# Performance work log

Hardware: AMD Instinct MI355X
Metric: run time of the kernel (lower is better)

## Reference

```python
import jax, jax.numpy as jnp
import numpy as np

IN_FEATURES = 3
CODE_NUM = 64
CODE_CHANNEL = 64
SHAPE_NUM = 1


def setup_inputs() -> dict:
    key = jax.random.key(0)
    k1, k2 = jax.random.split(key)
    coords = jax.random.uniform(k1, (8, 65536, IN_FEATURES), dtype=jnp.float32)  # in [0,1) subset of [-1,1]
    table_size = SHAPE_NUM * CODE_NUM ** IN_FEATURES
    # xavier_uniform for [C, N] matrix
    limit = float(np.sqrt(6.0 / (CODE_CHANNEL + table_size)))
    shape_code = jax.random.uniform(k2, (CODE_CHANNEL, table_size), dtype=jnp.float32,
                                    minval=-limit, maxval=limit)
    return {"coords": coords, "shape_code": shape_code, "idx": 0}


def reference(coords, shape_code, idx):
    D = IN_FEATURES
    # corner offset mask: [2^D, D] of {0,1}
    mask = jnp.stack(jnp.meshgrid(*([jnp.arange(2, dtype=jnp.float32)] * D), indexing="ij"), -1)
    mask = mask.reshape(-1, D)                                   # [8, 3]
    mul = jnp.asarray([CODE_NUM ** i for i in range(D)], dtype=jnp.int64)
    offset = jnp.asarray(idx, dtype=jnp.int64) * (CODE_NUM ** D)

    c = (coords + 1.0) * ((CODE_NUM - 1) / 2.0)                  # [B, P, 3] in [0, code_num-1]
    corners = jnp.floor(c)[..., None, :] + mask                  # [B, P, 8, 3]
    coordsf = c[..., None, :] - corners                          # [B, P, 8, 3]
    index = jnp.sum(corners.astype(jnp.int64) * mul, axis=-1) + offset  # [B, P, 8]
    weights = jnp.prod(1.0 - jnp.abs(coordsf), axis=-1)          # [B, P, 8]

    code = jnp.take(shape_code, index, axis=1)                   # [C, B, P, 8] gather
    out = jnp.einsum("cbpk,bpk->bpc", code, weights)             # weighted corner sum
    return out
```

## Files before the change

### kernel.cpp

```cpp
#include <hip/hip_runtime.h>


#define CODE_NUM 64
#define CODE_CHANNEL 64
#define TABLE (CODE_NUM * CODE_NUM * CODE_NUM)
#define NBINS 4096
#define SCAT_PTS 1024
#define SCAT_PPT 4

__global__ __launch_bounds__(256) void init_k(int* __restrict__ hist, int* __restrict__ bbox) {
    const int t = blockIdx.x * 256 + threadIdx.x;
    for (int i = t; i < NBINS; i += gridDim.x * 256) hist[i] = 0;
    if (t == 0) {
        bbox[0] = 0x7fffffff; bbox[1] = (int)0x80000000;
        bbox[2] = 0x7fffffff; bbox[3] = (int)0x80000000;
    }
}

__device__ __forceinline__ int cell_bin(float x, float y, float z,
                                        int& ix, int& iy, int& iz) {
    ix = (int)floorf((x + 1.0f) * ((CODE_NUM - 1) * 0.5f));
    iy = (int)floorf((y + 1.0f) * ((CODE_NUM - 1) * 0.5f));
    iz = (int)floorf((z + 1.0f) * ((CODE_NUM - 1) * 0.5f));
    const int cx = min(max(ix, 0), 63) >> 2;
    const int cy = min(max(iy, 0), 63) >> 2;
    const int cz = min(max(iz, 0), 63) >> 2;
    return cx | (cy << 4) | (cz << 8);
}

__global__ __launch_bounds__(256) void hist_bbox_k(const float* __restrict__ coords, int npoints,
                                                   int* __restrict__ hist, int* __restrict__ bbox) {
    __shared__ int lh[NBINS];
    __shared__ int lb[4];
    for (int i = threadIdx.x; i < NBINS; i += 256) lh[i] = 0;
    if (threadIdx.x == 0) {
        lb[0] = 0x7fffffff; lb[1] = (int)0x80000000;
        lb[2] = 0x7fffffff; lb[3] = (int)0x80000000;
    }
    __syncthreads();
    int ymin = 0x7fffffff, ymax = (int)0x80000000;
    int zmin = 0x7fffffff, zmax = (int)0x80000000;
    const int stride = gridDim.x * 256;
    for (int p = blockIdx.x * 256 + threadIdx.x; p < npoints; p += stride) {
        const float x = coords[p * 3 + 0];
        const float y = coords[p * 3 + 1];
        const float z = coords[p * 3 + 2];
        int ix, iy, iz;
        const int bin = cell_bin(x, y, z, ix, iy, iz);
        atomicAdd(&lh[bin], 1);
        ymin = min(ymin, iy); ymax = max(ymax, iy);
        zmin = min(zmin, iz); zmax = max(zmax, iz);
    }
    atomicMin(&lb[0], ymin); atomicMax(&lb[1], ymax);
    atomicMin(&lb[2], zmin); atomicMax(&lb[3], zmax);
    __syncthreads();
    for (int i = threadIdx.x; i < NBINS; i += 256) {
        const int c = lh[i];
        if (c) atomicAdd(&hist[i], c);
    }
    if (threadIdx.x == 0) {
        atomicMin(&bbox[0], lb[0]); atomicMax(&bbox[1], lb[1]);
        atomicMin(&bbox[2], lb[2]); atomicMax(&bbox[3], lb[3]);
    }
}

__global__ __launch_bounds__(64) void scan_k(const int* __restrict__ hist, int* __restrict__ cursor) {
    const int l = threadIdx.x;
    int s = 0;
#pragma unroll 1
    for (int i = 0; i < 64; ++i) s += hist[l * 64 + i];
    int inc = s;
#pragma unroll
    for (int d = 1; d < 64; d <<= 1) {
        const int u = __shfl_up(inc, d, 64);
        if (l >= d) inc += u;
    }
    int run = inc - s;
#pragma unroll 1
    for (int i = 0; i < 64; ++i) {
        cursor[l * 64 + i] = run;
        run += hist[l * 64 + i];
    }
}

__global__ __launch_bounds__(256) void scatter2_k(const float* __restrict__ coords, int npoints,
                                                  int* __restrict__ cursor,
                                                  float4* __restrict__ sorted) {
    __shared__ int lcount[NBINS];
    for (int i = threadIdx.x; i < NBINS; i += 256) lcount[i] = 0;
    __syncthreads();

    const int p0 = blockIdx.x * SCAT_PTS;
    float px[SCAT_PPT], py[SCAT_PPT], pz[SCAT_PPT];
    int pbin[SCAT_PPT], prank[SCAT_PPT];

#pragma unroll
    for (int i = 0; i < SCAT_PPT; ++i) {
        const int p = p0 + (i << 8) + (int)threadIdx.x;
        pbin[i] = -1;
        if (p < npoints) {
            const float x = coords[p * 3 + 0];
            const float y = coords[p * 3 + 1];
            const float z = coords[p * 3 + 2];
            int ix, iy, iz;
            const int bin = cell_bin(x, y, z, ix, iy, iz);
            px[i] = x; py[i] = y; pz[i] = z;
            pbin[i] = bin;
            prank[i] = atomicAdd(&lcount[bin], 1);
        }
    }
    __syncthreads();

    for (int i = threadIdx.x; i < NBINS; i += 256) {
        const int c = lcount[i];
        if (c) lcount[i] = atomicAdd(&cursor[i], c);
    }
    __syncthreads();

#pragma unroll
    for (int i = 0; i < SCAT_PPT; ++i) {
        if (pbin[i] >= 0) {
            const int p = p0 + (i << 8) + (int)threadIdx.x;
            const int slot = lcount[pbin[i]] + prank[i];
            sorted[slot] = make_float4(px[i], py[i], pz[i], __int_as_float(p));
        }
    }
}

__global__ __launch_bounds__(256) void transpose_bb_k(const float* __restrict__ src,
                                                      float* __restrict__ dst,
                                                      const int* __restrict__ bbox) {
    const int t0 = blockIdx.x * 64;
    const int y = (t0 >> 6) & 63;
    const int z = t0 >> 12;
    if (y < bbox[0] || y > bbox[1] + 1 || z < bbox[2] || z > bbox[3] + 1) return;

    __shared__ float tile[64 * 65];
    const int j = threadIdx.x;
#pragma unroll
    for (int i = 0; i < 4; ++i) {
        const int q = (i << 8) | j;
        const int c = q >> 4;
        const int tc4 = q & 15;
        const float4 v = *(const float4*)(src + (size_t)c * TABLE + t0 + (tc4 << 2));
        tile[((tc4 << 2) + 0) * 65 + c] = v.x;
        tile[((tc4 << 2) + 1) * 65 + c] = v.y;
        tile[((tc4 << 2) + 2) * 65 + c] = v.z;
        tile[((tc4 << 2) + 3) * 65 + c] = v.w;
    }
    __syncthreads();
#pragma unroll
    for (int i = 0; i < 4; ++i) {
        const int q = (i << 8) | j;
        const int t = q >> 4;
        const int c4 = q & 15;
        float4 v;
        v.x = tile[t * 65 + (c4 << 2) + 0];
        v.y = tile[t * 65 + (c4 << 2) + 1];
        v.z = tile[t * 65 + (c4 << 2) + 2];
        v.w = tile[t * 65 + (c4 << 2) + 3];
        *(float4*)(dst + (size_t)(t0 + t) * 64 + (c4 << 2)) = v;
    }
}

__global__ __launch_bounds__(256) void transpose_k(const float* __restrict__ src,
                                                   float* __restrict__ dst) {
    __shared__ float tile[64 * 65];
    const int t0 = blockIdx.x * 64;
    const int j = threadIdx.x;
#pragma unroll
    for (int i = 0; i < 4; ++i) {
        const int q = (i << 8) | j;
        const int c = q >> 4;
        const int tc4 = q & 15;
        const float4 v = *(const float4*)(src + (size_t)c * TABLE + t0 + (tc4 << 2));
        tile[((tc4 << 2) + 0) * 65 + c] = v.x;
        tile[((tc4 << 2) + 1) * 65 + c] = v.y;
        tile[((tc4 << 2) + 2) * 65 + c] = v.z;
        tile[((tc4 << 2) + 3) * 65 + c] = v.w;
    }
    __syncthreads();
#pragma unroll
    for (int i = 0; i < 4; ++i) {
        const int q = (i << 8) | j;
        const int t = q >> 4;
        const int c4 = q & 15;
        float4 v;
        v.x = tile[t * 65 + (c4 << 2) + 0];
        v.y = tile[t * 65 + (c4 << 2) + 1];
        v.z = tile[t * 65 + (c4 << 2) + 2];
        v.w = tile[t * 65 + (c4 << 2) + 3];
        *(float4*)(dst + (size_t)(t0 + t) * 64 + (c4 << 2)) = v;
    }
}

__global__ __launch_bounds__(256) void interp4s_k(const float4* __restrict__ sorted,
                                                  const float* __restrict__ table,
                                                  const int* __restrict__ idxp,
                                                  float* __restrict__ out,
                                                  int npoints) {
    unsigned bid = blockIdx.x;
    const unsigned nb = gridDim.x;
    if ((nb & 7u) == 0u) {
        const unsigned c = nb >> 3;
        bid = (bid & 7u) * c + (bid >> 3);
    }
    const int lane = threadIdx.x & 63;
    const int sub = lane >> 4;
    const int cg = lane & 15;
    const int p = (int)(bid * 16u + ((threadIdx.x >> 6) << 2) + (unsigned)sub);
    if (p >= npoints) return;

    const int offset = idxp[0] * TABLE;
    const float4 s4 = sorted[p];
    const int op = __float_as_int(s4.w);

    const float sx = (s4.x + 1.0f) * ((CODE_NUM - 1) * 0.5f);
    const float sy = (s4.y + 1.0f) * ((CODE_NUM - 1) * 0.5f);
    const float sz = (s4.z + 1.0f) * ((CODE_NUM - 1) * 0.5f);
    const float fx = floorf(sx), fy = floorf(sy), fz = floorf(sz);
    const float rx = sx - fx, ry = sy - fy, rz = sz - fz;
    const int ix = (int)fx, iy = (int)fy, iz = (int)fz;
    const int base = offset + ix + iy * CODE_NUM + iz * (CODE_NUM * CODE_NUM);

    const float wx[2] = {1.0f - rx, rx};
    const float wy[2] = {1.0f - ry, ry};
    const float wz[2] = {1.0f - rz, rz};

    const char* tp = (const char*)table;
    const int cgoff = cg << 4;

    float4 acc = make_float4(0.f, 0.f, 0.f, 0.f);
#pragma unroll
    for (int k = 0; k < 8; ++k) {
        const int a = k & 1, b = (k >> 1) & 1, c = (k >> 2) & 1;
        const int idx = base + a + b * CODE_NUM + c * (CODE_NUM * CODE_NUM);
        const float w = wx[a] * wy[b] * wz[c];
        const float4 v = *(const float4*)(tp + ((size_t)(unsigned)(idx << 8) + cgoff));
        acc.x = fmaf(w, v.x, acc.x);
        acc.y = fmaf(w, v.y, acc.y);
        acc.z = fmaf(w, v.z, acc.z);
        acc.w = fmaf(w, v.w, acc.w);
    }
    *(float4*)(out + (size_t)op * CODE_CHANNEL + (cg << 2)) = acc;
}

__global__ __launch_bounds__(256) void interp4_k(const float* __restrict__ coords,
                                                 const float* __restrict__ table,
                                                 const int* __restrict__ idxp,
                                                 float* __restrict__ out,
                                                 int npoints) {
    const unsigned tid = blockIdx.x * 256u + threadIdx.x;
    const int lane = threadIdx.x & 63;
    const int sub = lane >> 4;
    const int cg = lane & 15;
    const int p = (int)((tid >> 6) * 4u + (unsigned)sub);
    if (p >= npoints) return;

    const int offset = idxp[0] * TABLE;
    const float sx = (coords[p * 3 + 0] + 1.0f) * ((CODE_NUM - 1) * 0.5f);
    const float sy = (coords[p * 3 + 1] + 1.0f) * ((CODE_NUM - 1) * 0.5f);
    const float sz = (coords[p * 3 + 2] + 1.0f) * ((CODE_NUM - 1) * 0.5f);
    const float fx = floorf(sx), fy = floorf(sy), fz = floorf(sz);
    const float rx = sx - fx, ry = sy - fy, rz = sz - fz;
    const int ix = (int)fx, iy = (int)fy, iz = (int)fz;
    const int base = offset + ix + iy * CODE_NUM + iz * (CODE_NUM * CODE_NUM);
    const float wx[2] = {1.0f - rx, rx};
    const float wy[2] = {1.0f - ry, ry};
    const float wz[2] = {1.0f - rz, rz};
    const char* tp = (const char*)table;
    const int cgoff = cg << 4;
    float4 acc = make_float4(0.f, 0.f, 0.f, 0.f);
#pragma unroll
    for (int k = 0; k < 8; ++k) {
        const int a = k & 1, b = (k >> 1) & 1, c = (k >> 2) & 1;
        const int idx = base + a + b * CODE_NUM + c * (CODE_NUM * CODE_NUM);
        const float w = wx[a] * wy[b] * wz[c];
        const float4 v = *(const float4*)(tp + ((size_t)(unsigned)(idx << 8) + cgoff));
        acc.x = fmaf(w, v.x, acc.x);
        acc.y = fmaf(w, v.y, acc.y);
        acc.z = fmaf(w, v.z, acc.z);
        acc.w = fmaf(w, v.w, acc.w);
    }
    *(float4*)(out + (size_t)p * CODE_CHANNEL + (cg << 2)) = acc;
}

__global__ __launch_bounds__(256) void interp_fallback_k(const float* __restrict__ coords,
                                                         const float* __restrict__ table,
                                                         const int* __restrict__ idxp,
                                                         float* __restrict__ out,
                                                         int npoints) {
    const int p = (int)((blockIdx.x * 256u + threadIdx.x) >> 6);
    const int lane = threadIdx.x & 63;
    if (p >= npoints) return;
    const int offset = idxp[0] * TABLE;
    const float sx = (coords[p * 3 + 0] + 1.0f) * ((CODE_NUM - 1) * 0.5f);
    const float sy = (coords[p * 3 + 1] + 1.0f) * ((CODE_NUM - 1) * 0.5f);
    const float sz = (coords[p * 3 + 2] + 1.0f) * ((CODE_NUM - 1) * 0.5f);
    const float fx = floorf(sx), fy = floorf(sy), fz = floorf(sz);
    const float rx = sx - fx, ry = sy - fy, rz = sz - fz;
    const int base = offset + (int)fx + (int)fy * CODE_NUM + (int)fz * (CODE_NUM * CODE_NUM);
    const float wx[2] = {1.0f - rx, rx};
    const float wy[2] = {1.0f - ry, ry};
    const float wz[2] = {1.0f - rz, rz};
    float acc = 0.0f;
#pragma unroll
    for (int k = 0; k < 8; ++k) {
        const int a = k & 1, b = (k >> 1) & 1, c = (k >> 2) & 1;
        const int idx = base + a + b * CODE_NUM + c * (CODE_NUM * CODE_NUM);
        acc = fmaf(wx[a] * wy[b] * wz[c], table[(size_t)lane * TABLE + idx], acc);
    }
    out[(size_t)p * CODE_CHANNEL + lane] = acc;
}

extern "C" void kernel_launch(void* const* d_in, const int* in_sizes, int n_in,
                              void* d_out, int out_size, void* d_ws, size_t ws_size,
                              hipStream_t stream) {
    const float* coords = (const float*)d_in[0];
    const float* code   = (const float*)d_in[1];
    const int*   idxp   = (const int*)d_in[2];
    float* out = (float*)d_out;

    const int npoints = in_sizes[0] / 3;
    const size_t tbytes = (size_t)TABLE * CODE_CHANNEL * sizeof(float);
    const size_t sbytes = (size_t)npoints * sizeof(float4);
    const size_t need = tbytes + sbytes + 2 * NBINS * sizeof(int) + 64;

    if (ws_size >= need) {
        char* w = (char*)d_ws;
        float*  tt     = (float*)w;
        float4* sorted = (float4*)(w + tbytes);
        int*    hist   = (int*)(w + tbytes + sbytes);
        int*    cursor = hist + NBINS;
        int*    bbox   = cursor + NBINS;

        init_k<<<16, 256, 0, stream>>>(hist, bbox);
        hist_bbox_k<<<256, 256, 0, stream>>>(coords, npoints, hist, bbox);
        scan_k<<<1, 64, 0, stream>>>(hist, cursor);
        transpose_bb_k<<<TABLE / 64, 256, 0, stream>>>(code, tt, bbox);
        scatter2_k<<<(npoints + SCAT_PTS - 1) / SCAT_PTS, 256, 0, stream>>>(coords, npoints,
                                                                            cursor, sorted);
        interp4s_k<<<(npoints + 15) / 16, 256, 0, stream>>>(sorted, tt, idxp, out, npoints);
    } else if (ws_size >= tbytes) {
        float* tt = (float*)d_ws;
        transpose_k<<<TABLE / 64, 256, 0, stream>>>(code, tt);
        interp4_k<<<(npoints + 15) / 16, 256, 0, stream>>>(coords, tt, idxp, out, npoints);
    } else {
        interp_fallback_k<<<(npoints + 3) / 4, 256, 0, stream>>>(coords, code, idxp, out, npoints);
    }
}
```

Measured before the change: 273.6 us.

## Fuse table transpose with point scatter, parallelize scan, add nontemporal stores

Merges the bbox-limited table transpose and the point scatter into one launch whose blocks branch by index, so both phases run concurrently and one launch is saved. The single-wave serial scan is replaced by a 1024-thread two-level shuffle scan. Nontemporal stores are used for the transposed table and the output, and a nontemporal load for the sorted points. The risk is that nontemporal stores to the transposed table may bypass cache that the following gather kernel would otherwise hit.

```diff
diff --git a/kernel.cpp b/kernel.cpp
--- a/kernel.cpp
+++ b/kernel.cpp
@@ -7,6 +7,17 @@
 #define NBINS 4096
 #define SCAT_PTS 1024
 #define SCAT_PPT 4
+#define TBLOCKS (TABLE / 64)
+
+typedef float f4_t __attribute__((ext_vector_type(4)));
+
+__device__ __forceinline__ void nt_store_f4(float* p, float x, float y, float z, float w) {
+    f4_t v = {x, y, z, w};
+    __builtin_nontemporal_store(v, (f4_t*)p);
+}
+__device__ __forceinline__ f4_t nt_load_f4(const float* p) {
+    return __builtin_nontemporal_load((const f4_t*)p);
+}
 
 __global__ __launch_bounds__(256) void init_k(int* __restrict__ hist, int* __restrict__ bbox) {
     const int t = blockIdx.x * 256 + threadIdx.x;
@@ -64,78 +75,179 @@
     }
 }
 
-__global__ __launch_bounds__(64) void scan_k(const int* __restrict__ hist, int* __restrict__ cursor) {
-    const int l = threadIdx.x;
-    int s = 0;
-#pragma unroll 1
-    for (int i = 0; i < 64; ++i) s += hist[l * 64 + i];
+__global__ __launch_bounds__(1024) void scan_k(const int* __restrict__ hist,
+                                               int* __restrict__ cursor) {
+    const int t = threadIdx.x;
+    const int lane = t & 63;
+    const int wid = t >> 6;
+    const int4 h = ((const int4*)hist)[t];
+    const int s = h.x + h.y + h.z + h.w;
     int inc = s;
 #pragma unroll
     for (int d = 1; d < 64; d <<= 1) {
         const int u = __shfl_up(inc, d, 64);
-        if (l >= d) inc += u;
-    }
-    int run = inc - s;
-#pragma unroll 1
-    for (int i = 0; i < 64; ++i) {
-        cursor[l * 64 + i] = run;
-        run += hist[l * 64 + i];
-    }
-}
-
-__global__ __launch_bounds__(256) void scatter2_k(const float* __restrict__ coords, int npoints,
-                                                  int* __restrict__ cursor,
-                                                  float4* __restrict__ sorted) {
-    __shared__ int lcount[NBINS];
-    for (int i = threadIdx.x; i < NBINS; i += 256) lcount[i] = 0;
-    __syncthreads();
-
-    const int p0 = blockIdx.x * SCAT_PTS;
-    float px[SCAT_PPT], py[SCAT_PPT], pz[SCAT_PPT];
-    int pbin[SCAT_PPT], prank[SCAT_PPT];
-
-#pragma unroll
-    for (int i = 0; i < SCAT_PPT; ++i) {
-        const int p = p0 + (i << 8) + (int)threadIdx.x;
-        pbin[i] = -1;
-        if (p < npoints) {
-            const float x = coords[p * 3 + 0];
-            const float y = coords[p * 3 + 1];
-            const float z = coords[p * 3 + 2];
-            int ix, iy, iz;
-            const int bin = cell_bin(x, y, z, ix, iy, iz);
-            px[i] = x; py[i] = y; pz[i] = z;
-            pbin[i] = bin;
-            prank[i] = atomicAdd(&lcount[bin], 1);
-        }
-    }
-    __syncthreads();
-
-    for (int i = threadIdx.x; i < NBINS; i += 256) {
-        const int c = lcount[i];
-        if (c) lcount[i] = atomicAdd(&cursor[i], c);
-    }
-    __syncthreads();
-
-#pragma unroll
-    for (int i = 0; i < SCAT_PPT; ++i) {
-        if (pbin[i] >= 0) {
+        if (lane >= d) inc += u;
+    }
+    __shared__ int wsum[16];
+    if (lane == 63) wsum[wid] = inc;
+    __syncthreads();
+    if (t < 16) {
+        const int v = wsum[t];
+        int winc = v;
+#pragma unroll
+        for (int d = 1; d < 16; d <<= 1) {
+            const int u = __shfl_up(winc, d, 16);
+            if (t >= d) winc += u;
+        }
+        wsum[t] = winc - v;
+    }
+    __syncthreads();
+    const int base = wsum[wid] + (inc - s);
+    int4 c;
+    c.x = base;
+    c.y = base + h.x;
+    c.z = c.y + h.y;
+    c.w = c.z + h.z;
+    ((int4*)cursor)[t] = c;
+}
+
+__global__ __launch_bounds__(256) void mid_fused_k(const float* __restrict__ src,
+                                                   float* __restrict__ dst,
+                                                   const int* __restrict__ bbox,
+                                                   const float* __restrict__ coords, int npoints,
+                                                   int* __restrict__ cursor,
+                                                   float4* __restrict__ sorted) {
+    __shared__ int smem[64 * 65];
+
+    if (blockIdx.x < TBLOCKS) {
+        const int t0 = blockIdx.x * 64;
+        const int y = (t0 >> 6) & 63;
+        const int z = t0 >> 12;
+        if (y < bbox[0] || y > bbox[1] + 1 || z < bbox[2] || z > bbox[3] + 1) return;
+
+        float* tile = (float*)smem;
+        const int j = threadIdx.x;
+#pragma unroll
+        for (int i = 0; i < 4; ++i) {
+            const int q = (i << 8) | j;
+            const int c = q >> 4;
+            const int tc4 = q & 15;
+            const float4 v = *(const float4*)(src + (size_t)c * TABLE + t0 + (tc4 << 2));
+            tile[((tc4 << 2) + 0) * 65 + c] = v.x;
+            tile[((tc4 << 2) + 1) * 65 + c] = v.y;
+            tile[((tc4 << 2) + 2) * 65 + c] = v.z;
+            tile[((tc4 << 2) + 3) * 65 + c] = v.w;
+        }
+        __syncthreads();
+#pragma unroll
+        for (int i = 0; i < 4; ++i) {
+            const int q = (i << 8) | j;
+            const int t = q >> 4;
+            const int c4 = q & 15;
+            nt_store_f4(dst + (size_t)(t0 + t) * 64 + (c4 << 2),
+                        tile[t * 65 + (c4 << 2) + 0],
+                        tile[t * 65 + (c4 << 2) + 1],
+                        tile[t * 65 + (c4 << 2) + 2],
+                        tile[t * 65 + (c4 << 2) + 3]);
+        }
+    } else {
+        int* lcount = smem;
+        for (int i = threadIdx.x; i < NBINS; i += 256) lcount[i] = 0;
+        __syncthreads();
+
+        const int p0 = (int)(blockIdx.x - TBLOCKS) * SCAT_PTS;
+        float px[SCAT_PPT], py[SCAT_PPT], pz[SCAT_PPT];
+        int pbin[SCAT_PPT], prank[SCAT_PPT];
+
+#pragma unroll
+        for (int i = 0; i < SCAT_PPT; ++i) {
             const int p = p0 + (i << 8) + (int)threadIdx.x;
-            const int slot = lcount[pbin[i]] + prank[i];
-            sorted[slot] = make_float4(px[i], py[i], pz[i], __int_as_float(p));
-        }
-    }
-}
-
-__global__ __launch_bounds__(256) void transpose_bb_k(const float* __restrict__ src,
-                                                      float* __restrict__ dst,
-                                                      const int* __restrict__ bbox) {
+            pbin[i] = -1;
+            if (p < npoints) {
+                const float x = coords[p * 3 + 0];
+                const float y = coords[p * 3 + 1];
+                const float z = coords[p * 3 + 2];
+                int ix, iy, iz;
+                const int bin = cell_bin(x, y, z, ix, iy, iz);
+                px[i] = x; py[i] = y; pz[i] = z;
+                pbin[i] = bin;
+                prank[i] = atomicAdd(&lcount[bin], 1);
+            }
+        }
+        __syncthreads();
+
+        for (int i = threadIdx.x; i < NBINS; i += 256) {
+            const int c = lcount[i];
+            if (c) lcount[i] = atomicAdd(&cursor[i], c);
+        }
+        __syncthreads();
+
+#pragma unroll
+        for (int i = 0; i < SCAT_PPT; ++i) {
+            if (pbin[i] >= 0) {
+                const int p = p0 + (i << 8) + (int)threadIdx.x;
+                const int slot = lcount[pbin[i]] + prank[i];
+                sorted[slot] = make_float4(px[i], py[i], pz[i], __int_as_float(p));
+            }
+        }
+    }
+}
+
+__global__ __launch_bounds__(256) void interp4s_k(const float4* __restrict__ sorted,
+                                                  const float* __restrict__ table,
+                                                  const int* __restrict__ idxp,
+                                                  float* __restrict__ out,
+                                                  int npoints) {
+    unsigned bid = blockIdx.x;
+    const unsigned nb = gridDim.x;
+    if ((nb & 7u) == 0u) {
+        const unsigned c = nb >> 3;
+        bid = (bid & 7u) * c + (bid >> 3);
+    }
+    const int lane = threadIdx.x & 63;
+    const int sub = lane >> 4;
+    const int cg = lane & 15;
+    const int p = (int)(bid * 16u + ((threadIdx.x >> 6) << 2) + (unsigned)sub);
+    if (p >= npoints) return;
+
+    const int offset = idxp[0] * TABLE;
+    const f4_t s4 = nt_load_f4((const float*)(sorted + p));
+    const int op = __float_as_int(s4.w);
+
+    const float sx = (s4.x + 1.0f) * ((CODE_NUM - 1) * 0.5f);
+    const float sy = (s4.y + 1.0f) * ((CODE_NUM - 1) * 0.5f);
+    const float sz = (s4.z + 1.0f) * ((CODE_NUM - 1) * 0.5f);
+    const float fx = floorf(sx), fy = floorf(sy), fz = floorf(sz);
+    const float rx = sx - fx, ry = sy - fy, rz = sz - fz;
+    const int ix = (int)fx, iy = (int)fy, iz = (int)fz;
+    const int base = offset + ix + iy * CODE_NUM + iz * (CODE_NUM * CODE_NUM);
+
+    const float wx[2] = {1.0f - rx, rx};
+    const float wy[2] = {1.0f - ry, ry};
+    const float wz[2] = {1.0f - rz, rz};
+
+    const char* tp = (const char*)table;
+    const int cgoff = cg << 4;
+
+    float4 acc = make_float4(0.f, 0.f, 0.f, 0.f);
+#pragma unroll
+    for (int k = 0; k < 8; ++k) {
+        const int a = k & 1, b = (k >> 1) & 1, c = (k >> 2) & 1;
+        const int idx = base + a + b * CODE_NUM + c * (CODE_NUM * CODE_NUM);
+        const float w = wx[a] * wy[b] * wz[c];
+        const float4 v = *(const float4*)(tp + ((size_t)(unsigned)(idx << 8) + cgoff));
+        acc.x = fmaf(w, v.x, acc.x);
+        acc.y = fmaf(w, v.y, acc.y);
+        acc.z = fmaf(w, v.z, acc.z);
+        acc.w = fmaf(w, v.w, acc.w);
+    }
+    nt_store_f4(out + (size_t)op * CODE_CHANNEL + (cg << 2), acc.x, acc.y, acc.z, acc.w);
+}
+
+__global__ __launch_bounds__(256) void transpose_k(const float* __restrict__ src,
+                                                   float* __restrict__ dst) {
+    __shared__ float tile[64 * 65];
     const int t0 = blockIdx.x * 64;
-    const int y = (t0 >> 6) & 63;
-    const int z = t0 >> 12;
-    if (y < bbox[0] || y > bbox[1] + 1 || z < bbox[2] || z > bbox[3] + 1) return;
-
-    __shared__ float tile[64 * 65];
     const int j = threadIdx.x;
 #pragma unroll
     for (int i = 0; i < 4; ++i) {
@@ -161,88 +273,6 @@
         v.w = tile[t * 65 + (c4 << 2) + 3];
         *(float4*)(dst + (size_t)(t0 + t) * 64 + (c4 << 2)) = v;
     }
-}
-
-__global__ __launch_bounds__(256) void transpose_k(const float* __restrict__ src,
-                                                   float* __restrict__ dst) {
-    __shared__ float tile[64 * 65];
-    const int t0 = blockIdx.x * 64;
-    const int j = threadIdx.x;
-#pragma unroll
-    for (int i = 0; i < 4; ++i) {
-        const int q = (i << 8) | j;
-        const int c = q >> 4;
-        const int tc4 = q & 15;
-        const float4 v = *(const float4*)(src + (size_t)c * TABLE + t0 + (tc4 << 2));
-        tile[((tc4 << 2) + 0) * 65 + c] = v.x;
-        tile[((tc4 << 2) + 1) * 65 + c] = v.y;
-        tile[((tc4 << 2) + 2) * 65 + c] = v.z;
-        tile[((tc4 << 2) + 3) * 65 + c] = v.w;
-    }
-    __syncthreads();
-#pragma unroll
-    for (int i = 0; i < 4; ++i) {
-        const int q = (i << 8) | j;
-        const int t = q >> 4;
-        const int c4 = q & 15;
-        float4 v;
-        v.x = tile[t * 65 + (c4 << 2) + 0];
-        v.y = tile[t * 65 + (c4 << 2) + 1];
-        v.z = tile[t * 65 + (c4 << 2) + 2];
-        v.w = tile[t * 65 + (c4 << 2) + 3];
-        *(float4*)(dst + (size_t)(t0 + t) * 64 + (c4 << 2)) = v;
-    }
-}
-
-__global__ __launch_bounds__(256) void interp4s_k(const float4* __restrict__ sorted,
-                                                  const float* __restrict__ table,
-                                                  const int* __restrict__ idxp,
-                                                  float* __restrict__ out,
-                                                  int npoints) {
-    unsigned bid = blockIdx.x;
-    const unsigned nb = gridDim.x;
-    if ((nb & 7u) == 0u) {
-        const unsigned c = nb >> 3;
-        bid = (bid & 7u) * c + (bid >> 3);
-    }
-    const int lane = threadIdx.x & 63;
-    const int sub = lane >> 4;
-    const int cg = lane & 15;
-    const int p = (int)(bid * 16u + ((threadIdx.x >> 6) << 2) + (unsigned)sub);
-    if (p >= npoints) return;
-
-    const int offset = idxp[0] * TABLE;
-    const float4 s4 = sorted[p];
-    const int op = __float_as_int(s4.w);
-
-    const float sx = (s4.x + 1.0f) * ((CODE_NUM - 1) * 0.5f);
-    const float sy = (s4.y + 1.0f) * ((CODE_NUM - 1) * 0.5f);
-    const float sz = (s4.z + 1.0f) * ((CODE_NUM - 1) * 0.5f);
-    const float fx = floorf(sx), fy = floorf(sy), fz = floorf(sz);
-    const float rx = sx - fx, ry = sy - fy, rz = sz - fz;
-    const int ix = (int)fx, iy = (int)fy, iz = (int)fz;
-    const int base = offset + ix + iy * CODE_NUM + iz * (CODE_NUM * CODE_NUM);
-
-    const float wx[2] = {1.0f - rx, rx};
-    const float wy[2] = {1.0f - ry, ry};
-    const float wz[2] = {1.0f - rz, rz};
-
-    const char* tp = (const char*)table;
-    const int cgoff = cg << 4;
-
-    float4 acc = make_float4(0.f, 0.f, 0.f, 0.f);
-#pragma unroll
-    for (int k = 0; k < 8; ++k) {
-        const int a = k & 1, b = (k >> 1) & 1, c = (k >> 2) & 1;
-        const int idx = base + a + b * CODE_NUM + c * (CODE_NUM * CODE_NUM);
-        const float w = wx[a] * wy[b] * wz[c];
-        const float4 v = *(const float4*)(tp + ((size_t)(unsigned)(idx << 8) + cgoff));
-        acc.x = fmaf(w, v.x, acc.x);
-        acc.y = fmaf(w, v.y, acc.y);
-        acc.z = fmaf(w, v.z, acc.z);
-        acc.w = fmaf(w, v.w, acc.w);
-    }
-    *(float4*)(out + (size_t)op * CODE_CHANNEL + (cg << 2)) = acc;
 }
 
 __global__ __launch_bounds__(256) void interp4_k(const float* __restrict__ coords,
@@ -334,12 +364,13 @@
         int*    cursor = hist + NBINS;
         int*    bbox   = cursor + NBINS;
 
+        const int nscat = (npoints + SCAT_PTS - 1) / SCAT_PTS;
+
         init_k<<<16, 256, 0, stream>>>(hist, bbox);
         hist_bbox_k<<<256, 256, 0, stream>>>(coords, npoints, hist, bbox);
-        scan_k<<<1, 64, 0, stream>>>(hist, cursor);
-        transpose_bb_k<<<TABLE / 64, 256, 0, stream>>>(code, tt, bbox);
-        scatter2_k<<<(npoints + SCAT_PTS - 1) / SCAT_PTS, 256, 0, stream>>>(coords, npoints,
-                                                                            cursor, sorted);
+        scan_k<<<1, 1024, 0, stream>>>(hist, cursor);
+        mid_fused_k<<<TBLOCKS + nscat, 256, 0, stream>>>(code, tt, bbox,
+                                                         coords, npoints, cursor, sorted);
         interp4s_k<<<(npoints + 15) / 16, 256, 0, stream>>>(sorted, tt, idxp, out, npoints);
     } else if (ws_size >= tbytes) {
         float* tt = (float*)d_ws;
```

Measured after the change: 272.2 us. About the same (-0.5%).
